# Kernel optimization log

Hardware: AMD Instinct MI355X
Metric: run time of the kernel (lower is better)

Reference implementation:

```python
import jax, jax.numpy as jnp
import numpy as np

B, S, D_IN, D_OUT, H = 4, 2048, 1024, 1024, 16
HD = D_OUT // H


def setup_inputs() -> dict:
    key = jax.random.key(0)
    ks = jax.random.split(key, 6)
    s = 1.0 / np.sqrt(D_IN)
    x = jax.random.normal(ks[0], (B, S, D_IN), dtype=jnp.float32)
    Wq = jax.random.uniform(ks[1], (D_OUT, D_IN), jnp.float32, -s, s)  # torch Linear weight [out,in]
    Wk = jax.random.uniform(ks[2], (D_OUT, D_IN), jnp.float32, -s, s)
    Wv = jax.random.uniform(ks[3], (D_OUT, D_IN), jnp.float32, -s, s)
    so = 1.0 / np.sqrt(D_OUT)
    Wo = jax.random.uniform(ks[4], (D_OUT, D_OUT), jnp.float32, -so, so)
    bo = jax.random.uniform(ks[5], (D_OUT,), jnp.float32, -so, so)
    return {"x": x, "Wq": Wq, "Wk": Wk, "Wv": Wv, "Wo": Wo, "bo": bo}


def reference(x, Wq, Wk, Wv, Wo, bo):
    b, n, _ = x.shape
    # projections (torch Linear: x @ W^T), split heads -> [b, h, n, hd]
    def heads(y):
        return y.reshape(b, n, H, HD).transpose(0, 2, 1, 3)
    q = heads(x @ Wq.T)
    k = heads(x @ Wk.T)
    v = heads(x @ Wv.T)
    scores = jnp.einsum('bhqd,bhkd->bhqk', q, k)
    causal = jnp.triu(jnp.ones((n, n), dtype=bool), k=1)
    scores = jnp.where(causal, -jnp.inf, scores)
    attn = jax.nn.softmax(scores / np.sqrt(HD), axis=-1)  # dropout p=0.0 -> identity
    ctx = jnp.einsum('bhqk,bhkd->bhqd', attn, v)
    ctx = ctx.transpose(0, 2, 1, 3).reshape(b, n, D_OUT)
    return ctx @ Wo.T + bo
```

## Files before the change

kernel.cpp:

```cpp
#include <hip/hip_runtime.h>
#include <hip/hip_bf16.h>
#include <stdint.h>

#define B_N 4
#define SEQ 2048
#define DMODEL 1024
#define NHEAD 16
#define HDIM 64
#define BHEADS (B_N * NHEAD)
#define MROWS (B_N * SEQ)

typedef short bf16x8_t __attribute__((ext_vector_type(8)));
typedef float f32x4_t __attribute__((ext_vector_type(4)));

static __device__ __forceinline__ unsigned short f2bf(float f) {
  __hip_bfloat16 h = __float2bfloat16(f);
  return __builtin_bit_cast(unsigned short, h);
}

static __device__ __forceinline__ float fast_exp2(float x) {
  float r;
  asm("v_exp_f32 %0, %1" : "=v"(r) : "v"(x));
  return r;
}

#define GLDS16(gp, lp)                                                        \
  __builtin_amdgcn_global_load_lds(                                           \
      (const __attribute__((address_space(1))) unsigned int*)(gp),            \
      (__attribute__((address_space(3))) unsigned int*)(lp), 16, 0, 0)

__global__ void cast_all(const float* __restrict__ x,
                         const float* __restrict__ Wq,
                         const float* __restrict__ Wk,
                         const float* __restrict__ Wv,
                         const float* __restrict__ Wo,
                         unsigned short* __restrict__ out) {
  int i = blockIdx.x * blockDim.x + threadIdx.x;
  const int NX = (MROWS * DMODEL) / 4;
  const float* src;
  int off;
  float scale = 1.0f;
  if (i < NX) {
    src = x; off = i;
  } else {
    int j = i - NX;
    int mat = j >> 18;
    off = j & 262143;
    src = (mat == 0) ? Wq : (mat == 1) ? Wk : (mat == 2) ? Wv : Wo;
    if (mat == 0) scale = 0.18033688011112042f;
  }
  float4 v = reinterpret_cast<const float4*>(src)[off];
  ushort4 o;
  o.x = f2bf(v.x * scale); o.y = f2bf(v.y * scale);
  o.z = f2bf(v.z * scale); o.w = f2bf(v.w * scale);
  reinterpret_cast<ushort4*>(out)[i] = o;
}


#define SLOT_B 24576
#define NSLOTS 3

#define CERT(N)                                                               \
  asm volatile("s_waitcnt vmcnt(" #N ")" ::: "memory");                       \
  __builtin_amdgcn_s_barrier();                                               \
  asm volatile("" ::: "memory");

#define GEMM_PIPE_BODY                                                        \
  _Pragma("unroll")                                                           \
  for (int h = 0; h < 2; ++h) {                                               \
    char* sb = smem_c + h * SLOT_B;                                           \
    GLDS16(aB + (size_t)h * 32, sb + t * 16);                                 \
    GLDS16(b0B + (size_t)h * 32, sb + 8192 + t * 16);                         \
    GLDS16(b1B + (size_t)h * 32, sb + 16384 + t * 16);                        \
  }                                                                           \
  CERT(3)                                                                     \
  {                                                                           \
    int cur = 0, gs = 2;                                                      \
    const int NH = 32;                                                        \
    for (int h = 0; h < NH; ++h) {                                            \
      const char* cb = smem_c + cur * SLOT_B;                                 \
      bf16x8_t af[4], bfr[4];                                                 \
      _Pragma("unroll")                                                       \
      for (int rt = 0; rt < 4; rt++)                                          \
        af[rt] = *(const bf16x8_t*)(cb + offA[rt]);                           \
      _Pragma("unroll")                                                       \
      for (int ct = 0; ct < 4; ct++)                                          \
        bfr[ct] = *(const bf16x8_t*)(cb + offB[ct]);                          \
      if (h + 2 < NH) {                                                       \
        char* sb = smem_c + gs * SLOT_B;                                      \
        GLDS16(aB + (size_t)(h + 2) * 32, sb + t * 16);                       \
        GLDS16(b0B + (size_t)(h + 2) * 32, sb + 8192 + t * 16);               \
        GLDS16(b1B + (size_t)(h + 2) * 32, sb + 16384 + t * 16);              \
      }                                                                       \
      __builtin_amdgcn_s_setprio(1);                                          \
      _Pragma("unroll")                                                       \
      for (int rt = 0; rt < 4; rt++)                                          \
        _Pragma("unroll")                                                     \
        for (int ct = 0; ct < 4; ct++)                                        \
          acc[rt][ct] = __builtin_amdgcn_mfma_f32_16x16x32_bf16(              \
              af[rt], bfr[ct], acc[rt][ct], 0, 0, 0);                         \
      __builtin_amdgcn_s_setprio(0);                                          \
      if (h + 1 < NH) {                                                       \
        if (h + 2 < NH) { CERT(3) } else { CERT(0) }                          \
      }                                                                       \
      if (++cur == NSLOTS) cur = 0;                                           \
      if (++gs == NSLOTS) gs = 0;                                             \
    }                                                                         \
  }

__global__ __launch_bounds__(512, 4)
void gemm_qkv(const unsigned short* __restrict__ A,
              const unsigned short* __restrict__ W,
              unsigned short* __restrict__ Out) {
  __shared__ __align__(16) unsigned short smem[36864];
  char* smem_c = (char*)smem;

  const int t = threadIdx.x;
  const int lane = t & 63;
  const int w = t >> 6;
  const int quad = lane >> 4;
  const int l16 = lane & 15;
  const int rowBase = blockIdx.x * 128;
  const int colBase = blockIdx.y * 256;
  const int wr = (w >> 2) * 64;
  const int wc = (w & 3) * 64;
  const int K = DMODEL;

  const int srow = t >> 2;
  const int ssw = ((t & 3) ^ ((t >> 3) & 3)) * 8;
  const unsigned short* aB  = A + (size_t)(rowBase + srow) * K + ssw;
  const unsigned short* b0B = W + (size_t)(colBase + srow) * K + ssw;
  const unsigned short* b1B = W + (size_t)(colBase + 128 + srow) * K + ssw;

  const int swz = (quad ^ ((l16 >> 1) & 3)) * 16;
  int offA[4], offB[4];
#pragma unroll
  for (int rt = 0; rt < 4; rt++) offA[rt] = (wr + rt * 16 + l16) * 64 + swz;
#pragma unroll
  for (int ct = 0; ct < 4; ct++)
    offB[ct] = 8192 + (wc + ct * 16 + l16) * 64 + swz;

  f32x4_t zero4 = {0.f, 0.f, 0.f, 0.f};
  f32x4_t acc[4][4];
#pragma unroll
  for (int i = 0; i < 4; i++)
#pragma unroll
    for (int j = 0; j < 4; j++) acc[i][j] = zero4;

  GEMM_PIPE_BODY

  __syncthreads();

  const int mat = colBase >> 10;
  const int nl = colBase & 1023;
  const int hh = (nl + wc) >> 6;
  const int bb = rowBase >> 11;

  if (mat == 2) {
    unsigned short* T = smem + w * 4608;
#pragma unroll
    for (int ct = 0; ct < 4; ct++)
#pragma unroll
      for (int rt = 0; rt < 4; rt++) {
        ushort4 pk;
        pk.x = f2bf(acc[rt][ct][0]);
        pk.y = f2bf(acc[rt][ct][1]);
        pk.z = f2bf(acc[rt][ct][2]);
        pk.w = f2bf(acc[rt][ct][3]);
        *(ushort4*)&T[(ct * 16 + l16) * 72 + rt * 16 + quad * 4] = pk;
      }
    const int srw = (rowBase & (SEQ - 1)) + wr;
    unsigned short* Cq = Out + 2 * (size_t)MROWS * DMODEL;
#pragma unroll
    for (int it = 0; it < 8; it++) {
      int nn = it * 8 + (lane >> 3);
      int sg = lane & 7;
      uint4 d = *(const uint4*)&T[nn * 72 + sg * 8];
      *(uint4*)(Cq + ((size_t)(bb * NHEAD + hh) * HDIM + nn) * SEQ + srw +
                sg * 8) = d;
    }
  } else {
    unsigned short* T = smem + w * 4608;
#pragma unroll
    for (int rt = 0; rt < 4; rt++)
#pragma unroll
      for (int ct = 0; ct < 4; ct++)
#pragma unroll
        for (int r = 0; r < 4; r++)
          T[(rt * 16 + quad * 4 + r) * 72 + ct * 16 + l16] =
              f2bf(acc[rt][ct][r]);
    unsigned short* Cq = Out + (size_t)mat * MROWS * DMODEL;
#pragma unroll
    for (int it = 0; it < 8; it++) {
      int idx = it * 64 + lane;
      int row = idx >> 3, sg = idx & 7, sgx = sg ^ (row & 7);
      uint4 d = *(const uint4*)&T[row * 72 + sgx * 8];
      int m = rowBase + wr + row;
      int s = m & (SEQ - 1), b = m >> 11;
      *(uint4*)(Cq + (((size_t)(b * NHEAD + hh)) * SEQ + s) * HDIM + sgx * 8) = d;
    }
  }
}

__global__ __launch_bounds__(512, 4)
void gemm_out(const unsigned short* __restrict__ A,
              const unsigned short* __restrict__ Bw,
              float* __restrict__ Cf, const float* __restrict__ bias) {
  __shared__ __align__(16) unsigned short smem[36864];
  char* smem_c = (char*)smem;

  const int t = threadIdx.x;
  const int lane = t & 63;
  const int w = t >> 6;
  const int quad = lane >> 4;
  const int l16 = lane & 15;
  const int rowBase = blockIdx.x * 128;
  const int colBase = blockIdx.y * 256;
  const int wr = (w >> 2) * 64;
  const int wc = (w & 3) * 64;
  const int K = DMODEL, N = DMODEL;

  const int srow = t >> 2;
  const int ssw = ((t & 3) ^ ((t >> 3) & 3)) * 8;
  const unsigned short* aB  = A + (size_t)(rowBase + srow) * K + ssw;
  const unsigned short* b0B = Bw + (size_t)(colBase + srow) * K + ssw;
  const unsigned short* b1B = Bw + (size_t)(colBase + 128 + srow) * K + ssw;

  const int swz = (quad ^ ((l16 >> 1) & 3)) * 16;
  int offA[4], offB[4];
#pragma unroll
  for (int rt = 0; rt < 4; rt++) offA[rt] = (wr + rt * 16 + l16) * 64 + swz;
#pragma unroll
  for (int ct = 0; ct < 4; ct++)
    offB[ct] = 8192 + (wc + ct * 16 + l16) * 64 + swz;

  f32x4_t zero4 = {0.f, 0.f, 0.f, 0.f};
  f32x4_t acc[4][4];
#pragma unroll
  for (int i = 0; i < 4; i++)
#pragma unroll
    for (int j = 0; j < 4; j++) acc[i][j] = zero4;

  GEMM_PIPE_BODY

#pragma unroll
  for (int rt = 0; rt < 4; rt++)
#pragma unroll
    for (int ct = 0; ct < 4; ct++) {
      int n = colBase + wc + ct * 16 + l16;
      float bv = bias[n];
#pragma unroll
      for (int r = 0; r < 4; r++) {
        int m = rowBase + wr + rt * 16 + quad * 4 + r;
        Cf[(size_t)m * N + n] = acc[rt][ct][r] + bv;
      }
    }
}

__global__ __launch_bounds__(256, 3)
void attn_kernel(const unsigned short* __restrict__ Qg_,
                 const unsigned short* __restrict__ Kg_,
                 const unsigned short* __restrict__ Vtg_,
                 unsigned short* __restrict__ ctx) {
  __shared__ __align__(16) unsigned short Ks[2][4096];
  __shared__ __align__(16) unsigned short Vs[2][4096];
  __shared__ __align__(16) unsigned short Ps[4][2048];

  const int t = threadIdx.x;
  const int lane = t & 63, w = t >> 6;
  const int quad = lane >> 4, l16 = lane & 15;
  const int sw = l16 & 7;
  unsigned short* PsW = &Ps[w][0];

  const int rank = blockIdx.x;
  const int qt = 15 - (rank >> 6);
  const int bh = rank & 63;
  const int nt = 2 * qt + 2;
  const size_t base = (size_t)bh * SEQ * HDIM;

  const int r0 = t >> 3;
  const int s0 = ((t & 7) ^ (r0 & 7)) * 8;
  const int r1 = r0 + 32;

  const unsigned short* Kg = Kg_ + base;
  const unsigned short* Vg = Vtg_ + base;

  GLDS16(Kg + r0 * HDIM + s0, (char*)&Ks[0][0] + t * 16);
  GLDS16(Kg + r1 * HDIM + s0, (char*)&Ks[0][0] + t * 16 + 4096);
  GLDS16(Vg + (size_t)r0 * SEQ + s0, (char*)&Vs[0][0] + t * 16);
  GLDS16(Vg + (size_t)r1 * SEQ + s0, (char*)&Vs[0][0] + t * 16 + 4096);

  const int q0w = qt * 128 + w * 32;

  bf16x8_t qf[2][2];
#pragma unroll
  for (int q2 = 0; q2 < 2; q2++)
#pragma unroll
    for (int kh = 0; kh < 2; kh++)
      qf[q2][kh] = *(const bf16x8_t*)(Qg_ + base +
          (size_t)(q0w + q2 * 16 + l16) * HDIM + kh * 32 + quad * 8);

  float l_[2] = {0.f, 0.f};
  f32x4_t zero4 = {0.f, 0.f, 0.f, 0.f};
  f32x4_t o[2][4];
#pragma unroll
  for (int q2 = 0; q2 < 2; q2++)
#pragma unroll
    for (int dt = 0; dt < 4; dt++) o[q2][dt] = zero4;

  int buf = 0;
  for (int jt = 0; jt < nt; ++jt) {
    __syncthreads();
    if (jt + 1 < nt) {
      const unsigned short* Kg2 = Kg + (size_t)(jt + 1) * 64 * HDIM;
      const unsigned short* Vg2 = Vg + (jt + 1) * 64;
      char* kd = (char*)&Ks[buf ^ 1][0] + t * 16;
      char* vd = (char*)&Vs[buf ^ 1][0] + t * 16;
      GLDS16(Kg2 + r0 * HDIM + s0, kd);
      GLDS16(Kg2 + r1 * HDIM + s0, kd + 4096);
      GLDS16(Vg2 + (size_t)r0 * SEQ + s0, vd);
      GLDS16(Vg2 + (size_t)r1 * SEQ + s0, vd + 4096);
    }

    if (jt * 64 <= q0w + 31) {
      const unsigned short* Kb = &Ks[buf][0];
      const unsigned short* Vb = &Vs[buf][0];
      f32x4_t sc[2][4];
#pragma unroll
      for (int q2 = 0; q2 < 2; q2++)
#pragma unroll
        for (int kt = 0; kt < 4; kt++) sc[q2][kt] = zero4;

#pragma unroll
      for (int kt = 0; kt < 4; kt++)
#pragma unroll
        for (int kh = 0; kh < 2; kh++) {
          bf16x8_t kf = *(const bf16x8_t*)((const char*)Kb +
              ((kt * 16 + l16) * 64 + (((kh * 4 + quad) ^ sw) * 8)) * 2);
          sc[0][kt] = __builtin_amdgcn_mfma_f32_16x16x32_bf16(
              kf, qf[0][kh], sc[0][kt], 0, 0, 0);
          sc[1][kt] = __builtin_amdgcn_mfma_f32_16x16x32_bf16(
              kf, qf[1][kh], sc[1][kt], 0, 0, 0);
        }

      if (jt * 64 + 63 > q0w) {
#pragma unroll
        for (int q2 = 0; q2 < 2; q2++) {
          int q = q0w + q2 * 16 + l16;
#pragma unroll
          for (int kt = 0; kt < 4; kt++)
#pragma unroll
            for (int r = 0; r < 4; r++) {
              int key = jt * 64 + kt * 16 + quad * 4 + r;
              if (key > q) sc[q2][kt][r] = -3.0e38f;
            }
        }
      }

#pragma unroll
      for (int q2 = 0; q2 < 2; q2++) {
        float sum = 0.f;
#pragma unroll
        for (int kt = 0; kt < 4; kt++) {
          float p0 = fast_exp2(sc[q2][kt][0]);
          float p1 = fast_exp2(sc[q2][kt][1]);
          float p2 = fast_exp2(sc[q2][kt][2]);
          float p3 = fast_exp2(sc[q2][kt][3]);
          sum += p0 + p1 + p2 + p3;
          ushort4 pk;
          pk.x = f2bf(p0); pk.y = f2bf(p1); pk.z = f2bf(p2); pk.w = f2bf(p3);
          int u = (kt * 4 + quad) ^ ((l16 & 7) << 1);
          *(ushort4*)&PsW[q2 * 1024 + l16 * 64 + u * 4] = pk;
        }
        sum += __shfl_xor(sum, 16, 64);
        sum += __shfl_xor(sum, 32, 64);
        l_[q2] += sum;
      }

      bf16x8_t pf[2][2];
#pragma unroll
      for (int q2 = 0; q2 < 2; q2++)
#pragma unroll
        for (int kc = 0; kc < 2; kc++) {
          int u = (kc * 8 + quad * 2) ^ ((l16 & 7) << 1);
          pf[q2][kc] = *(const bf16x8_t*)&PsW[q2 * 1024 + l16 * 64 + u * 4];
        }
#pragma unroll
      for (int dt = 0; dt < 4; dt++)
#pragma unroll
        for (int kc = 0; kc < 2; kc++) {
          bf16x8_t vfrag = *(const bf16x8_t*)((const char*)Vb +
              ((dt * 16 + l16) * 64 + (((kc * 4 + quad) ^ sw) * 8)) * 2);
          o[0][dt] = __builtin_amdgcn_mfma_f32_16x16x32_bf16(
              vfrag, pf[0][kc], o[0][dt], 0, 0, 0);
          o[1][dt] = __builtin_amdgcn_mfma_f32_16x16x32_bf16(
              vfrag, pf[1][kc], o[1][dt], 0, 0, 0);
        }
    }
    buf ^= 1;
  }

  const int bidx = bh >> 4, h = bh & 15;
#pragma unroll
  for (int q2 = 0; q2 < 2; q2++) {
    float inv = 1.0f / l_[q2];
#pragma unroll
    for (int dt = 0; dt < 4; dt++) {
      ushort4 pk;
      pk.x = f2bf(o[q2][dt][0] * inv);
      pk.y = f2bf(o[q2][dt][1] * inv);
      pk.z = f2bf(o[q2][dt][2] * inv);
      pk.w = f2bf(o[q2][dt][3] * inv);
      int u = (dt * 4 + quad) ^ ((l16 & 7) << 1);
      *(ushort4*)&PsW[q2 * 1024 + l16 * 64 + u * 4] = pk;
    }
  }
  {
    int qq = lane >> 2, sg = lane & 3;
#pragma unroll
    for (int q2 = 0; q2 < 2; q2++) {
      int ua = (sg * 2) ^ ((qq & 7) << 1);
      int ub = (sg * 2 + 8) ^ ((qq & 7) << 1);
      uint4 da = *(const uint4*)&PsW[q2 * 1024 + qq * 64 + ua * 4];
      uint4 db = *(const uint4*)&PsW[q2 * 1024 + qq * 64 + ub * 4];
      size_t rowoff =
          ((size_t)(bidx * SEQ + q0w + q2 * 16 + qq)) * DMODEL + h * HDIM;
      *(uint4*)(ctx + rowoff + sg * 8) = da;
      *(uint4*)(ctx + rowoff + (sg + 4) * 8) = db;
    }
  }
}

extern "C" void kernel_launch(void* const* d_in, const int* in_sizes, int n_in,
                              void* d_out, int out_size, void* d_ws,
                              size_t ws_size, hipStream_t stream) {
  const float* x  = (const float*)d_in[0];
  const float* Wq = (const float*)d_in[1];
  const float* Wk = (const float*)d_in[2];
  const float* Wv = (const float*)d_in[3];
  const float* Wo = (const float*)d_in[4];
  const float* bo = (const float*)d_in[5];
  float* out = (float*)d_out;

  const size_t XE = (size_t)MROWS * DMODEL;
  const size_t WE = (size_t)DMODEL * DMODEL;

  unsigned short* xb   = (unsigned short*)d_ws;
  unsigned short* wqb  = xb + XE;
  unsigned short* wob  = wqb + 3 * WE;
  unsigned short* Qb   = wqb + 4 * WE;
  unsigned short* Kb   = Qb + XE;
  unsigned short* Vtb  = Kb + XE;
  unsigned short* ctxb = xb;

  cast_all<<<(int)((XE / 4 + WE) / 256), 256, 0, stream>>>(x, Wq, Wk, Wv, Wo,
                                                           xb);

  gemm_qkv<<<dim3(MROWS / 128, 3 * DMODEL / 256), 512, 0, stream>>>(xb, wqb, Qb);

  attn_kernel<<<dim3(1024), 256, 0, stream>>>(Qb, Kb, Vtb, ctxb);

  gemm_out<<<dim3(MROWS / 128, DMODEL / 256), 512, 0, stream>>>(ctxb, wob, out, bo);
}
```

Before: 222.6 us.

## Split long causal attention query tiles across two blocks with a combine pass

Query tiles 8-15, the ones with the most key blocks under the causal mask, now have their key range split in half across two workgroups. Each half writes unnormalized fp32 partial outputs and row sums to workspace, and a new combine kernel adds the halves, normalizes and writes bf16 context. The aim is to cut the tail of the causal workload imbalance and give the GPU more blocks to schedule. In exchange it adds an extra kernel launch and fp32 partial traffic. It only activates when the workspace is large enough. The partial merge adds the halves without a max rescale, which relies on the existing softmax using a fixed or shared offset.

Result: slower. 240.8 us (+8.2%).

```diff
diff --git a/kernel.cpp b/kernel.cpp
--- a/kernel.cpp
+++ b/kernel.cpp
@@ -261,7 +261,9 @@
 void attn_kernel(const unsigned short* __restrict__ Qg_,
                  const unsigned short* __restrict__ Kg_,
                  const unsigned short* __restrict__ Vtg_,
-                 unsigned short* __restrict__ ctx) {
+                 unsigned short* __restrict__ ctx,
+                 float* __restrict__ Op, float* __restrict__ Lp,
+                 int do_split) {
   __shared__ __align__(16) unsigned short Ks[2][4096];
   __shared__ __align__(16) unsigned short Vs[2][4096];
   __shared__ __align__(16) unsigned short Ps[4][2048];
@@ -273,9 +275,19 @@
   unsigned short* PsW = &Ps[w][0];
 
   const int rank = blockIdx.x;
-  const int qt = 15 - (rank >> 6);
-  const int bh = rank & 63;
-  const int nt = 2 * qt + 2;
+  int qt, bh, j0, j1, c = 0, split = 0;
+  if (do_split && rank < 1024) {
+    int idx = rank >> 1; c = rank & 1;
+    qt = 15 - (idx >> 6); bh = idx & 63;
+    int half = qt + 1;
+    j0 = c ? half : 0; j1 = c ? (2 * qt + 2) : half;
+    split = 1;
+  } else {
+    int rr = do_split ? (rank - 1024) : rank;
+    qt = do_split ? (7 - (rr >> 6)) : (15 - (rr >> 6));
+    bh = rr & 63;
+    j0 = 0; j1 = 2 * qt + 2;
+  }
   const size_t base = (size_t)bh * SEQ * HDIM;
 
   const int r0 = t >> 3;
@@ -285,10 +297,14 @@
   const unsigned short* Kg = Kg_ + base;
   const unsigned short* Vg = Vtg_ + base;
 
-  GLDS16(Kg + r0 * HDIM + s0, (char*)&Ks[0][0] + t * 16);
-  GLDS16(Kg + r1 * HDIM + s0, (char*)&Ks[0][0] + t * 16 + 4096);
-  GLDS16(Vg + (size_t)r0 * SEQ + s0, (char*)&Vs[0][0] + t * 16);
-  GLDS16(Vg + (size_t)r1 * SEQ + s0, (char*)&Vs[0][0] + t * 16 + 4096);
+  {
+    const unsigned short* Kg0 = Kg + (size_t)j0 * 64 * HDIM;
+    const unsigned short* Vg0 = Vg + j0 * 64;
+    GLDS16(Kg0 + r0 * HDIM + s0, (char*)&Ks[0][0] + t * 16);
+    GLDS16(Kg0 + r1 * HDIM + s0, (char*)&Ks[0][0] + t * 16 + 4096);
+    GLDS16(Vg0 + (size_t)r0 * SEQ + s0, (char*)&Vs[0][0] + t * 16);
+    GLDS16(Vg0 + (size_t)r1 * SEQ + s0, (char*)&Vs[0][0] + t * 16 + 4096);
+  }
 
   const int q0w = qt * 128 + w * 32;
 
@@ -309,9 +325,9 @@
     for (int dt = 0; dt < 4; dt++) o[q2][dt] = zero4;
 
   int buf = 0;
-  for (int jt = 0; jt < nt; ++jt) {
+  for (int jt = j0; jt < j1; ++jt) {
     __syncthreads();
-    if (jt + 1 < nt) {
+    if (jt + 1 < j1) {
       const unsigned short* Kg2 = Kg + (size_t)(jt + 1) * 64 * HDIM;
       const unsigned short* Vg2 = Vg + (jt + 1) * 64;
       char* kd = (char*)&Ks[buf ^ 1][0] + t * 16;
@@ -400,35 +416,73 @@
     buf ^= 1;
   }
 
-  const int bidx = bh >> 4, h = bh & 15;
-#pragma unroll
-  for (int q2 = 0; q2 < 2; q2++) {
-    float inv = 1.0f / l_[q2];
-#pragma unroll
-    for (int dt = 0; dt < 4; dt++) {
-      ushort4 pk;
-      pk.x = f2bf(o[q2][dt][0] * inv);
-      pk.y = f2bf(o[q2][dt][1] * inv);
-      pk.z = f2bf(o[q2][dt][2] * inv);
-      pk.w = f2bf(o[q2][dt][3] * inv);
-      int u = (dt * 4 + quad) ^ ((l16 & 7) << 1);
-      *(ushort4*)&PsW[q2 * 1024 + l16 * 64 + u * 4] = pk;
-    }
-  }
-  {
-    int qq = lane >> 2, sg = lane & 3;
+  if (split) {
+    const int si = (15 - qt) * 64 + bh;
+    float* Ob = Op + ((size_t)(c * 512 + si) * 128) * 64;
+    float* Lb = Lp + (size_t)(c * 512 + si) * 128;
 #pragma unroll
     for (int q2 = 0; q2 < 2; q2++) {
-      int ua = (sg * 2) ^ ((qq & 7) << 1);
-      int ub = (sg * 2 + 8) ^ ((qq & 7) << 1);
-      uint4 da = *(const uint4*)&PsW[q2 * 1024 + qq * 64 + ua * 4];
-      uint4 db = *(const uint4*)&PsW[q2 * 1024 + qq * 64 + ub * 4];
-      size_t rowoff =
-          ((size_t)(bidx * SEQ + q0w + q2 * 16 + qq)) * DMODEL + h * HDIM;
-      *(uint4*)(ctx + rowoff + sg * 8) = da;
-      *(uint4*)(ctx + rowoff + (sg + 4) * 8) = db;
-    }
-  }
+      int lr = w * 32 + q2 * 16 + l16;
+#pragma unroll
+      for (int dt = 0; dt < 4; dt++)
+        *(f32x4_t*)&Ob[(size_t)lr * 64 + dt * 16 + quad * 4] = o[q2][dt];
+      if (quad == 0) Lb[lr] = l_[q2];
+    }
+  } else {
+    const int bidx = bh >> 4, h = bh & 15;
+#pragma unroll
+    for (int q2 = 0; q2 < 2; q2++) {
+      float inv = 1.0f / l_[q2];
+#pragma unroll
+      for (int dt = 0; dt < 4; dt++) {
+        ushort4 pk;
+        pk.x = f2bf(o[q2][dt][0] * inv);
+        pk.y = f2bf(o[q2][dt][1] * inv);
+        pk.z = f2bf(o[q2][dt][2] * inv);
+        pk.w = f2bf(o[q2][dt][3] * inv);
+        int u = (dt * 4 + quad) ^ ((l16 & 7) << 1);
+        *(ushort4*)&PsW[q2 * 1024 + l16 * 64 + u * 4] = pk;
+      }
+    }
+    {
+      int qq = lane >> 2, sg = lane & 3;
+#pragma unroll
+      for (int q2 = 0; q2 < 2; q2++) {
+        int ua = (sg * 2) ^ ((qq & 7) << 1);
+        int ub = (sg * 2 + 8) ^ ((qq & 7) << 1);
+        uint4 da = *(const uint4*)&PsW[q2 * 1024 + qq * 64 + ua * 4];
+        uint4 db = *(const uint4*)&PsW[q2 * 1024 + qq * 64 + ub * 4];
+        size_t rowoff =
+            ((size_t)(bidx * SEQ + q0w + q2 * 16 + qq)) * DMODEL + h * HDIM;
+        *(uint4*)(ctx + rowoff + sg * 8) = da;
+        *(uint4*)(ctx + rowoff + (sg + 4) * 8) = db;
+      }
+    }
+  }
+}
+
+__global__ void attn_combine(const float* __restrict__ Op,
+                             const float* __restrict__ Lp,
+                             unsigned short* __restrict__ ctx) {
+  int gid = blockIdx.x * 256 + threadIdx.x;
+  int si = gid >> 11;
+  int rem = gid & 2047;
+  int lr = rem >> 4;
+  int d4 = (rem & 15) * 4;
+  size_t o0 = ((size_t)si * 128 + lr) * 64 + d4;
+  size_t o1 = ((size_t)(512 + si) * 128 + lr) * 64 + d4;
+  float4 a = *(const float4*)&Op[o0];
+  float4 b = *(const float4*)&Op[o1];
+  float l = Lp[si * 128 + lr] + Lp[(512 + si) * 128 + lr];
+  float inv = 1.0f / l;
+  ushort4 o;
+  o.x = f2bf((a.x + b.x) * inv);
+  o.y = f2bf((a.y + b.y) * inv);
+  o.z = f2bf((a.z + b.z) * inv);
+  o.w = f2bf((a.w + b.w) * inv);
+  int qt = 15 - (si >> 6), bh = si & 63, bidx = bh >> 4, h = bh & 15;
+  *(ushort4*)(ctx + ((size_t)(bidx * SEQ) + qt * 128 + lr) * DMODEL +
+              h * HDIM + d4) = o;
 }
 
 extern "C" void kernel_launch(void* const* d_in, const int* in_sizes, int n_in,
@@ -444,6 +498,8 @@
 
   const size_t XE = (size_t)MROWS * DMODEL;
   const size_t WE = (size_t)DMODEL * DMODEL;
+  const size_t OP_ELEMS = (size_t)2 * 512 * 128 * 64;
+  const size_t LP_ELEMS = (size_t)2 * 512 * 128;
 
   unsigned short* xb   = (unsigned short*)d_ws;
   unsigned short* wqb  = xb + XE;
@@ -452,13 +508,21 @@
   unsigned short* Kb   = Qb + XE;
   unsigned short* Vtb  = Kb + XE;
   unsigned short* ctxb = xb;
+  float* Op = (float*)(Vtb + XE);
+  float* Lp = Op + OP_ELEMS;
+
+  const size_t need = (4 * XE + 4 * WE) * 2 + (OP_ELEMS + LP_ELEMS) * 4;
+  const int do_split = (ws_size >= need) ? 1 : 0;
 
   cast_all<<<(int)((XE / 4 + WE) / 256), 256, 0, stream>>>(x, Wq, Wk, Wv, Wo,
                                                            xb);
 
   gemm_qkv<<<dim3(MROWS / 128, 3 * DMODEL / 256), 512, 0, stream>>>(xb, wqb, Qb);
 
-  attn_kernel<<<dim3(1024), 256, 0, stream>>>(Qb, Kb, Vtb, ctxb);
+  attn_kernel<<<dim3(do_split ? 1536 : 1024), 256, 0, stream>>>(
+      Qb, Kb, Vtb, ctxb, Op, Lp, do_split);
+  if (do_split)
+    attn_combine<<<dim3(4096), 256, 0, stream>>>(Op, Lp, ctxb);
 
   gemm_out<<<dim3(MROWS / 128, DMODEL / 256), 512, 0, stream>>>(ctxb, wob, out, bo);
 }
```

## Enlarge QKV GEMM tile to 256x256 with double-buffered BK=64 pipeline

Applied to the files above, without the earlier changes.

Rewrites the QKV projection GEMM main loop to use 256x256 output tiles per block, with each wave computing 128x64. The new loop runs a two-buffer LDS pipeline with 64-wide K steps, splitting the global-to-LDS prefetch of A and B between the first two of four MFMA phases separated by barriers. This aims to raise arithmetic intensity and reduce global/LDS traffic per FLOP. In exchange it uses 128KB of LDS and twice the accumulators, which limits occupancy to one block per CU. The grid also drops to 384 blocks, which may leave a partial tail wave.

Result: no change. 226.0 us (+1.5%).

```diff
diff --git a/kernel.cpp b/kernel.cpp
--- a/kernel.cpp
+++ b/kernel.cpp
@@ -108,46 +108,156 @@
     }                                                                         \
   }
 
-__global__ __launch_bounds__(512, 4)
+__global__ __launch_bounds__(512, 2)
 void gemm_qkv(const unsigned short* __restrict__ A,
               const unsigned short* __restrict__ W,
               unsigned short* __restrict__ Out) {
-  __shared__ __align__(16) unsigned short smem[36864];
-  char* smem_c = (char*)smem;
+  __shared__ __align__(16) unsigned short smem[65536];
 
   const int t = threadIdx.x;
   const int lane = t & 63;
   const int w = t >> 6;
   const int quad = lane >> 4;
   const int l16 = lane & 15;
-  const int rowBase = blockIdx.x * 128;
+  const int rowBase = blockIdx.x * 256;
   const int colBase = blockIdx.y * 256;
-  const int wr = (w >> 2) * 64;
+  const int wr = (w >> 2) * 128;
   const int wc = (w & 3) * 64;
   const int K = DMODEL;
 
-  const int srow = t >> 2;
-  const int ssw = ((t & 3) ^ ((t >> 3) & 3)) * 8;
-  const unsigned short* aB  = A + (size_t)(rowBase + srow) * K + ssw;
-  const unsigned short* b0B = W + (size_t)(colBase + srow) * K + ssw;
-  const unsigned short* b1B = W + (size_t)(colBase + 128 + srow) * K + ssw;
-
-  const int swz = (quad ^ ((l16 >> 1) & 3)) * 16;
-  int offA[4], offB[4];
-#pragma unroll
-  for (int rt = 0; rt < 4; rt++) offA[rt] = (wr + rt * 16 + l16) * 64 + swz;
-#pragma unroll
-  for (int ct = 0; ct < 4; ct++)
-    offB[ct] = 8192 + (wc + ct * 16 + l16) * 64 + swz;
+  const int ssw = ((t & 7) ^ ((t >> 4) & 7)) * 8;
+  const unsigned short* aRow = A + (size_t)(rowBase + (t >> 3)) * K + ssw;
+  const unsigned short* bRow = W + (size_t)(colBase + (t >> 3)) * K + ssw;
+
+  const int sx = (l16 >> 1) & 7;
+  int rA[8], cB[4], kgr[2];
+#pragma unroll
+  for (int rt = 0; rt < 8; rt++) rA[rt] = (wr + rt * 16 + l16) * 128;
+#pragma unroll
+  for (int ct = 0; ct < 4; ct++) cB[ct] = 32768 + (wc + ct * 16 + l16) * 128;
+#pragma unroll
+  for (int kk = 0; kk < 2; kk++) kgr[kk] = ((kk * 4 + quad) ^ sx) * 16;
 
   f32x4_t zero4 = {0.f, 0.f, 0.f, 0.f};
-  f32x4_t acc[4][4];
-#pragma unroll
-  for (int i = 0; i < 4; i++)
+  f32x4_t acc[8][4];
+#pragma unroll
+  for (int i = 0; i < 8; i++)
 #pragma unroll
     for (int j = 0; j < 4; j++) acc[i][j] = zero4;
 
-  GEMM_PIPE_BODY
+  {
+    char* nb = (char*)smem;
+    GLDS16(aRow, nb + t * 16);
+    GLDS16(aRow + (size_t)64 * K, nb + 8192 + t * 16);
+    GLDS16(aRow + (size_t)128 * K, nb + 16384 + t * 16);
+    GLDS16(aRow + (size_t)192 * K, nb + 24576 + t * 16);
+    GLDS16(bRow, nb + 32768 + t * 16);
+    GLDS16(bRow + (size_t)64 * K, nb + 40960 + t * 16);
+    GLDS16(bRow + (size_t)128 * K, nb + 49152 + t * 16);
+    GLDS16(bRow + (size_t)192 * K, nb + 57344 + t * 16);
+  }
+  asm volatile("s_waitcnt vmcnt(0)" ::: "memory");
+  __builtin_amdgcn_s_barrier();
+
+  for (int kt = 0; kt < 16; ++kt) {
+    const char* cb = (const char*)smem + (size_t)(kt & 1) * 65536;
+    char* nb = (char*)smem + (size_t)((kt & 1) ^ 1) * 65536;
+    const int kn = (kt + 1) * 64;
+    const bool pf = (kt + 1 < 16);
+
+    bf16x8_t bfr[4][2];
+    bf16x8_t afp[2][2];
+
+#pragma unroll
+    for (int ct = 0; ct < 4; ct++)
+#pragma unroll
+      for (int kk = 0; kk < 2; kk++)
+        bfr[ct][kk] = *(const bf16x8_t*)(cb + cB[ct] + kgr[kk]);
+#pragma unroll
+    for (int rp = 0; rp < 2; rp++)
+#pragma unroll
+      for (int kk = 0; kk < 2; kk++)
+        afp[rp][kk] = *(const bf16x8_t*)(cb + rA[rp] + kgr[kk]);
+    if (pf) {
+      GLDS16(aRow + kn, nb + t * 16);
+      GLDS16(aRow + (size_t)64 * K + kn, nb + 8192 + t * 16);
+      GLDS16(aRow + (size_t)128 * K + kn, nb + 16384 + t * 16);
+      GLDS16(aRow + (size_t)192 * K + kn, nb + 24576 + t * 16);
+    }
+    __builtin_amdgcn_s_barrier();
+    __builtin_amdgcn_s_setprio(1);
+#pragma unroll
+    for (int rp = 0; rp < 2; rp++)
+#pragma unroll
+      for (int ct = 0; ct < 4; ct++)
+#pragma unroll
+        for (int kk = 0; kk < 2; kk++)
+          acc[rp][ct] = __builtin_amdgcn_mfma_f32_16x16x32_bf16(
+              afp[rp][kk], bfr[ct][kk], acc[rp][ct], 0, 0, 0);
+    __builtin_amdgcn_s_setprio(0);
+    __builtin_amdgcn_s_barrier();
+
+#pragma unroll
+    for (int rp = 0; rp < 2; rp++)
+#pragma unroll
+      for (int kk = 0; kk < 2; kk++)
+        afp[rp][kk] = *(const bf16x8_t*)(cb + rA[2 + rp] + kgr[kk]);
+    if (pf) {
+      GLDS16(bRow + kn, nb + 32768 + t * 16);
+      GLDS16(bRow + (size_t)64 * K + kn, nb + 40960 + t * 16);
+      GLDS16(bRow + (size_t)128 * K + kn, nb + 49152 + t * 16);
+      GLDS16(bRow + (size_t)192 * K + kn, nb + 57344 + t * 16);
+    }
+    __builtin_amdgcn_s_barrier();
+    __builtin_amdgcn_s_setprio(1);
+#pragma unroll
+    for (int rp = 0; rp < 2; rp++)
+#pragma unroll
+      for (int ct = 0; ct < 4; ct++)
+#pragma unroll
+        for (int kk = 0; kk < 2; kk++)
+          acc[2 + rp][ct] = __builtin_amdgcn_mfma_f32_16x16x32_bf16(
+              afp[rp][kk], bfr[ct][kk], acc[2 + rp][ct], 0, 0, 0);
+    __builtin_amdgcn_s_setprio(0);
+    __builtin_amdgcn_s_barrier();
+
+#pragma unroll
+    for (int rp = 0; rp < 2; rp++)
+#pragma unroll
+      for (int kk = 0; kk < 2; kk++)
+        afp[rp][kk] = *(const bf16x8_t*)(cb + rA[4 + rp] + kgr[kk]);
+    __builtin_amdgcn_s_barrier();
+    __builtin_amdgcn_s_setprio(1);
+#pragma unroll
+    for (int rp = 0; rp < 2; rp++)
+#pragma unroll
+      for (int ct = 0; ct < 4; ct++)
+#pragma unroll
+        for (int kk = 0; kk < 2; kk++)
+          acc[4 + rp][ct] = __builtin_amdgcn_mfma_f32_16x16x32_bf16(
+              afp[rp][kk], bfr[ct][kk], acc[4 + rp][ct], 0, 0, 0);
+    __builtin_amdgcn_s_setprio(0);
+    __builtin_amdgcn_s_barrier();
+
+#pragma unroll
+    for (int rp = 0; rp < 2; rp++)
+#pragma unroll
+      for (int kk = 0; kk < 2; kk++)
+        afp[rp][kk] = *(const bf16x8_t*)(cb + rA[6 + rp] + kgr[kk]);
+    __builtin_amdgcn_s_barrier();
+    __builtin_amdgcn_s_setprio(1);
+#pragma unroll
+    for (int rp = 0; rp < 2; rp++)
+#pragma unroll
+      for (int ct = 0; ct < 4; ct++)
+#pragma unroll
+        for (int kk = 0; kk < 2; kk++)
+          acc[6 + rp][ct] = __builtin_amdgcn_mfma_f32_16x16x32_bf16(
+              afp[rp][kk], bfr[ct][kk], acc[6 + rp][ct], 0, 0, 0);
+    __builtin_amdgcn_s_setprio(0);
+    if (pf) asm volatile("s_waitcnt vmcnt(0)" ::: "memory");
+    __builtin_amdgcn_s_barrier();
+  }
 
   __syncthreads();
 
@@ -158,46 +268,53 @@
 
   if (mat == 2) {
     unsigned short* T = smem + w * 4608;
-#pragma unroll
-    for (int ct = 0; ct < 4; ct++)
-#pragma unroll
-      for (int rt = 0; rt < 4; rt++) {
-        ushort4 pk;
-        pk.x = f2bf(acc[rt][ct][0]);
-        pk.y = f2bf(acc[rt][ct][1]);
-        pk.z = f2bf(acc[rt][ct][2]);
-        pk.w = f2bf(acc[rt][ct][3]);
-        *(ushort4*)&T[(ct * 16 + l16) * 72 + rt * 16 + quad * 4] = pk;
+    unsigned short* Cq = Out + 2 * (size_t)MROWS * DMODEL;
+#pragma unroll
+    for (int s = 0; s < 2; s++) {
+#pragma unroll
+      for (int ct = 0; ct < 4; ct++)
+#pragma unroll
+        for (int rt = 0; rt < 4; rt++) {
+          ushort4 pk;
+          pk.x = f2bf(acc[s * 4 + rt][ct][0]);
+          pk.y = f2bf(acc[s * 4 + rt][ct][1]);
+          pk.z = f2bf(acc[s * 4 + rt][ct][2]);
+          pk.w = f2bf(acc[s * 4 + rt][ct][3]);
+          *(ushort4*)&T[(ct * 16 + l16) * 72 + rt * 16 + quad * 4] = pk;
+        }
+      const int srw = (rowBase & (SEQ - 1)) + wr + s * 64;
+#pragma unroll
+      for (int it = 0; it < 8; it++) {
+        int nn = it * 8 + (lane >> 3);
+        int sg = lane & 7;
+        uint4 d = *(const uint4*)&T[nn * 72 + sg * 8];
+        *(uint4*)(Cq + ((size_t)(bb * NHEAD + hh) * HDIM + nn) * SEQ + srw +
+                  sg * 8) = d;
       }
-    const int srw = (rowBase & (SEQ - 1)) + wr;
-    unsigned short* Cq = Out + 2 * (size_t)MROWS * DMODEL;
-#pragma unroll
-    for (int it = 0; it < 8; it++) {
-      int nn = it * 8 + (lane >> 3);
-      int sg = lane & 7;
-      uint4 d = *(const uint4*)&T[nn * 72 + sg * 8];
-      *(uint4*)(Cq + ((size_t)(bb * NHEAD + hh) * HDIM + nn) * SEQ + srw +
-                sg * 8) = d;
     }
   } else {
     unsigned short* T = smem + w * 4608;
-#pragma unroll
-    for (int rt = 0; rt < 4; rt++)
-#pragma unroll
-      for (int ct = 0; ct < 4; ct++)
-#pragma unroll
-        for (int r = 0; r < 4; r++)
-          T[(rt * 16 + quad * 4 + r) * 72 + ct * 16 + l16] =
-              f2bf(acc[rt][ct][r]);
     unsigned short* Cq = Out + (size_t)mat * MROWS * DMODEL;
 #pragma unroll
-    for (int it = 0; it < 8; it++) {
-      int idx = it * 64 + lane;
-      int row = idx >> 3, sg = idx & 7, sgx = sg ^ (row & 7);
-      uint4 d = *(const uint4*)&T[row * 72 + sgx * 8];
-      int m = rowBase + wr + row;
-      int s = m & (SEQ - 1), b = m >> 11;
-      *(uint4*)(Cq + (((size_t)(b * NHEAD + hh)) * SEQ + s) * HDIM + sgx * 8) = d;
+    for (int s = 0; s < 2; s++) {
+#pragma unroll
+      for (int rt = 0; rt < 4; rt++)
+#pragma unroll
+        for (int ct = 0; ct < 4; ct++)
+#pragma unroll
+          for (int r = 0; r < 4; r++)
+            T[(rt * 16 + quad * 4 + r) * 72 + ct * 16 + l16] =
+                f2bf(acc[s * 4 + rt][ct][r]);
+#pragma unroll
+      for (int it = 0; it < 8; it++) {
+        int idx = it * 64 + lane;
+        int row = idx >> 3, sg = idx & 7, sgx = sg ^ (row & 7);
+        uint4 d = *(const uint4*)&T[row * 72 + sgx * 8];
+        int m = rowBase + wr + s * 64 + row;
+        int sq = m & (SEQ - 1), b = m >> 11;
+        *(uint4*)(Cq + (((size_t)(b * NHEAD + hh)) * SEQ + sq) * HDIM +
+                  sgx * 8) = d;
+      }
     }
   }
 }
@@ -456,7 +573,7 @@
   cast_all<<<(int)((XE / 4 + WE) / 256), 256, 0, stream>>>(x, Wq, Wk, Wv, Wo,
                                                            xb);
 
-  gemm_qkv<<<dim3(MROWS / 128, 3 * DMODEL / 256), 512, 0, stream>>>(xb, wqb, Qb);
+  gemm_qkv<<<dim3(MROWS / 256, 3 * DMODEL / 256), 512, 0, stream>>>(xb, wqb, Qb);
 
   attn_kernel<<<dim3(1024), 256, 0, stream>>>(Qb, Kb, Vtb, ctxb);
 
```
